# Kernel optimization log

Measured on AMD Instinct MI355X. Metric: run time of the kernel, lower is better.

The kernel has to match this reference:

```python
import jax, jax.numpy as jnp
import numpy as np

N_ITERS = 2
N_NODES = 50000
N_EDGES = 400000
NODE_DIM = 128
EDGE_DIM = 128
MLP_HIDDEN = 128


def _gru_cell(x, h, W_ih, W_hh, b_ih, b_hh):
    # torch.nn.GRUCell math. W_ih: [3H, in], W_hh: [3H, H]
    gi = x @ W_ih.T + b_ih
    gh = h @ W_hh.T + b_hh
    i_r, i_z, i_n = jnp.split(gi, 3, axis=-1)
    h_r, h_z, h_n = jnp.split(gh, 3, axis=-1)
    r = jax.nn.sigmoid(i_r + h_r)
    z = jax.nn.sigmoid(i_z + h_z)
    n = jnp.tanh(i_n + r * h_n)
    return (1.0 - z) * n + z * h


def _edge_softmax(logits, dst, num_nodes):
    # logits: [E], normalized over incoming edges of each dst node
    m = jax.ops.segment_max(logits, dst, num_segments=num_nodes)
    e = jnp.exp(logits - m[dst])
    s = jax.ops.segment_sum(e, dst, num_segments=num_nodes)
    return e / s[dst]


def setup_inputs() -> dict:
    key = jax.random.key(0)
    ks = jax.random.split(key, 20)
    s = 0.05
    inp = {
        'nf': jax.random.normal(ks[0], (N_NODES, NODE_DIM), jnp.float32),
        'ef': jax.random.normal(ks[1], (N_EDGES, EDGE_DIM), jnp.float32),
        'src': jax.random.randint(ks[2], (N_EDGES,), 0, N_NODES, jnp.int32),
        'dst': jax.random.randint(ks[3], (N_EDGES,), 0, N_NODES, jnp.int32),
        # edge GRUCell: input 2*node_dim -> hidden edge_dim
        'eW_ih': s * jax.random.normal(ks[4], (3 * EDGE_DIM, 2 * NODE_DIM), jnp.float32),
        'eW_hh': s * jax.random.normal(ks[5], (3 * EDGE_DIM, EDGE_DIM), jnp.float32),
        'eb_ih': s * jax.random.normal(ks[6], (3 * EDGE_DIM,), jnp.float32),
        'eb_hh': s * jax.random.normal(ks[7], (3 * EDGE_DIM,), jnp.float32),
        # node GRUCell: input edge_dim -> hidden node_dim
        'nW_ih': s * jax.random.normal(ks[8], (3 * NODE_DIM, EDGE_DIM), jnp.float32),
        'nW_hh': s * jax.random.normal(ks[9], (3 * NODE_DIM, NODE_DIM), jnp.float32),
        'nb_ih': s * jax.random.normal(ks[10], (3 * NODE_DIM,), jnp.float32),
        'nb_hh': s * jax.random.normal(ks[11], (3 * NODE_DIM,), jnp.float32),
        # attention MLP: edge_dim -> hidden -> 1
        'aW1': s * jax.random.normal(ks[12], (EDGE_DIM, MLP_HIDDEN), jnp.float32),
        'ab1': jnp.zeros((MLP_HIDDEN,), jnp.float32),
        'aW2': s * jax.random.normal(ks[13], (MLP_HIDDEN, 1), jnp.float32),
        'ab2': jnp.zeros((1,), jnp.float32),
    }
    return inp


def reference(nf, ef, src, dst, eW_ih, eW_hh, eb_ih, eb_hh,
              nW_ih, nW_hh, nb_ih, nb_hh, aW1, ab1, aW2, ab2):
    num_nodes = nf.shape[0]
    for _ in range(N_ITERS):
        # per-edge GRU update: input = [src_h ; dst_h], hidden = edge feature
        x_e = jnp.concatenate([nf[src], nf[dst]], axis=-1)  # [E, 2*node_dim]
        uef = _gru_cell(x_e, ef, eW_ih, eW_hh, eb_ih, eb_hh)  # [E, edge_dim]
        # attention MLP + edge softmax over destination neighborhoods
        logits = (jax.nn.relu(uef @ aW1 + ab1) @ aW2 + ab2)[:, 0]  # [E]
        attn = _edge_softmax(logits, dst, num_nodes)  # [E]
        # weighted scatter-sum aggregation to destination nodes
        agg_m = jax.ops.segment_sum(uef * attn[:, None], dst, num_segments=num_nodes)
        # node GRU update
        unf = _gru_cell(agg_m, nf, nW_ih, nW_hh, nb_ih, nb_hh)  # [N, node_dim]
        nf, ef = unf, uef
    return (nf, ef)
```

## Files before the change

kernel.cpp:

```cpp
#include <hip/hip_runtime.h>

#define NN 50000
#define NE 400000
#define DIM 128

typedef __bf16 bf16x8 __attribute__((ext_vector_type(8)));
typedef float f32x4 __attribute__((ext_vector_type(4)));
typedef unsigned short u16;

#define MFMA16 __builtin_amdgcn_mfma_f32_16x16x32_bf16

__device__ __forceinline__ u16 f2b(float f){ __bf16 b=(__bf16)f; return __builtin_bit_cast(u16,b); }
__device__ __forceinline__ float b2f(u16 h){ unsigned u = ((unsigned)h)<<16; return __builtin_bit_cast(float,u); }
__device__ __forceinline__ float sigm(float x){ return 1.0f/(1.0f+__expf(-x)); }
__device__ __forceinline__ float tanh_(float x){ float e=__expf(2.0f*x); return 1.0f-2.0f/(e+1.0f); }
__device__ __forceinline__ bf16x8 ldb8(const u16* p){ return *reinterpret_cast<const bf16x8*>(p); }

#define GLOAD_LDS(gp, lp) __builtin_amdgcn_global_load_lds( \
    (const __attribute__((address_space(1))) void*)(gp),    \
    (__attribute__((address_space(3))) void*)(lp), 16, 0, 0)

__global__ void f2b_kernel(const float* __restrict__ in, u16* __restrict__ out, int n4){
  int i = blockIdx.x*blockDim.x + threadIdx.x;
  int st = gridDim.x*blockDim.x;
  for (; i<n4; i+=st){
    float4 v = reinterpret_cast<const float4*>(in)[i];
    ushort4 o = { f2b(v.x), f2b(v.y), f2b(v.z), f2b(v.w) };
    reinterpret_cast<ushort4*>(out)[i] = o;
  }
}

__global__ void transpose128_kernel(const float* __restrict__ in, u16* __restrict__ out){
  int i = blockIdx.x*blockDim.x + threadIdx.x;
  int k = i>>7, n = i&127;
  out[n*128+k] = f2b(in[i]);
}

__global__ void zero_kernel(int* p, int n){
  int i = blockIdx.x*blockDim.x + threadIdx.x; if (i<n) p[i]=0;
}
__global__ void hist_kernel(const int* __restrict__ dst, int* __restrict__ counts, int n){
  int i = blockIdx.x*blockDim.x + threadIdx.x; if (i<n) atomicAdd(&counts[dst[i]],1);
}
__global__ void scan_kernel(const int* __restrict__ counts, int* __restrict__ rowp,
                            int* __restrict__ cursor, int n){
  __shared__ int buf[1024];
  __shared__ int run;
  const int t = threadIdx.x;
  if (t==0) run = 0;
  __syncthreads();
  for (int base=0; base<n; base+=1024){
    int v = (base+t<n) ? counts[base+t] : 0;
    buf[t]=v; __syncthreads();
    for (int off=1; off<1024; off<<=1){
      int x = (t>=off) ? buf[t-off] : 0;
      __syncthreads();
      buf[t]+=x; __syncthreads();
    }
    int incl = buf[t];
    int br = run;
    __syncthreads();
    if (base+t<n){ int ex = br+incl-v; rowp[base+t]=ex; cursor[base+t]=ex; }
    if (t==1023) run = br+incl;
    __syncthreads();
  }
  if (t==0) rowp[n]=run;
}
__global__ void scatter_kernel(const int* __restrict__ dst, int* __restrict__ cursor,
                               int* __restrict__ eids, int n){
  int i = blockIdx.x*blockDim.x + threadIdx.x;
  if (i<n){ int p = atomicAdd(&cursor[dst[i]],1); eids[p]=i; }
}

__global__ __launch_bounds__(256, 2)
void edge_kernel(const int* __restrict__ src, const int* __restrict__ dst,
                 const u16* __restrict__ nfb, u16* __restrict__ efb,
                 const u16* __restrict__ Wih, const u16* __restrict__ Whh,
                 const float* __restrict__ bih, const float* __restrict__ bhh,
                 const u16* __restrict__ aW1T, const float* __restrict__ ab1,
                 const float* __restrict__ aW2, const float* __restrict__ ab2,
                 float* __restrict__ logits, float* __restrict__ ef32out)
{
  __shared__ __align__(16) u16 wbuf[36*512];
  const int wave = threadIdx.x>>6, lane = threadIdx.x&63;
  const int r16 = lane&15, kq = lane>>4;
  const long base = (long)blockIdx.x*128 + wave*32;

  auto stage = [&](int c){
    if (c < 8){
      for (int f = wave; f < 36; f += 4){
        const u16* g;
        if (f < 24){ const int gt = f>>3, s = f&7;
          g = Wih + (long)(gt*128 + c*16 + r16)*256 + s*32 + kq*8; }
        else { const int q = f-24, gt = q>>2, s = q&3;
          g = Whh + (long)(gt*128 + c*16 + r16)*128 + s*32 + kq*8; }
        GLOAD_LDS(g, wbuf + f*512);
      }
    } else {
      for (int f = wave; f < 32; f += 4){
        const int t = f>>2, s = f&3;
        GLOAD_LDS(aW1T + (long)(t*16 + r16)*128 + s*32 + kq*8, wbuf + f*512);
      }
    }
  };

  bf16x8 ag[2][8], ae[2][4];
#pragma unroll
  for (int m=0;m<2;++m){
    const long e = base + m*16 + r16;
    const u16* sp = nfb + (long)src[e]*DIM;
    const u16* dp = nfb + (long)dst[e]*DIM;
    const u16* ep = efb + e*DIM;
#pragma unroll
    for (int s=0;s<4;++s){
      ag[m][s]   = ldb8(sp + s*32 + kq*8);
      ag[m][s+4] = ldb8(dp + s*32 + kq*8);
      ae[m][s]   = ldb8(ep + s*32 + kq*8);
    }
  }
  stage(0);
  __syncthreads();

  u16*  ebase = efb + (base + kq*4)*DIM + r16;
  float* fbase = ef32out ? ef32out + (base + kq*4)*DIM + r16 : nullptr;
  const float* bi0 = bih + r16;
  const float* bh0 = bhh + r16;

  const f32x4 vzero = {0.f,0.f,0.f,0.f};
  const u16* lbase = wbuf + lane*8;

#pragma unroll 1
  for (int c=0;c<8;++c){
    const int c16 = c*16;
    const float bir=bi0[c16], biz=bi0[c16+DIM], bin=bi0[c16+2*DIM];
    const float bhr=bh0[c16], bhz=bh0[c16+DIM], bhn=bh0[c16+2*DIM];
    float h0p[2][4];
#pragma unroll
    for (int m=0;m<2;++m)
#pragma unroll
      for (int r=0;r<4;++r) h0p[m][r] = b2f(ebase[(m*16+r)*DIM + c16]);

    f32x4 aR[2], aZ[2], aNi[2], aNh[2];
#pragma unroll
    for (int m=0;m<2;++m){ aR[m]=vzero; aZ[m]=vzero; aNi[m]=vzero; aNh[m]=vzero; }
#pragma unroll
    for (int s=0;s<8;++s){
      bf16x8 b0 = ldb8(lbase + ( s   )*512);
      bf16x8 b1 = ldb8(lbase + ( 8+s )*512);
      bf16x8 b2 = ldb8(lbase + (16+s )*512);
#pragma unroll
      for (int m=0;m<2;++m){
        aR[m]  = MFMA16(ag[m][s], b0, aR[m] ,0,0,0);
        aZ[m]  = MFMA16(ag[m][s], b1, aZ[m] ,0,0,0);
        aNi[m] = MFMA16(ag[m][s], b2, aNi[m],0,0,0);
      }
    }
#pragma unroll
    for (int s=0;s<4;++s){
      bf16x8 b0 = ldb8(lbase + (24+s)*512);
      bf16x8 b1 = ldb8(lbase + (28+s)*512);
      bf16x8 b2 = ldb8(lbase + (32+s)*512);
#pragma unroll
      for (int m=0;m<2;++m){
        aR[m]  = MFMA16(ae[m][s], b0, aR[m] ,0,0,0);
        aZ[m]  = MFMA16(ae[m][s], b1, aZ[m] ,0,0,0);
        aNh[m] = MFMA16(ae[m][s], b2, aNh[m],0,0,0);
      }
    }
    __syncthreads();
    stage(c+1);
#pragma unroll
    for (int m=0;m<2;++m){
#pragma unroll
      for (int r=0;r<4;++r){
        float rg = sigm(aR[m][r] + bir + bhr);
        float zg = sigm(aZ[m][r] + biz + bhz);
        float ng = tanh_(aNi[m][r] + bin + rg*(aNh[m][r] + bhn));
        float u  = (1.0f-zg)*ng + zg*h0p[m][r];
        ebase[(m*16+r)*DIM + c16] = f2b(u);
        if (fbase) fbase[(m*16+r)*DIM + c16] = u;
      }
    }
    __syncthreads();
  }

  bf16x8 ua[2][4];
#pragma unroll
  for (int m=0;m<2;++m){
    const u16* ep = efb + (base + m*16 + r16)*DIM;
#pragma unroll
    for (int s=0;s<4;++s) ua[m][s] = ldb8(ep + s*32 + kq*8);
  }
  float part[2][4] = {{0.f,0.f,0.f,0.f},{0.f,0.f,0.f,0.f}};
#pragma unroll 1
  for (int t=0;t<8;++t){
    f32x4 h[2] = {vzero, vzero};
#pragma unroll
    for (int s=0;s<4;++s){
      bf16x8 b = ldb8(lbase + (t*4+s)*512);
#pragma unroll
      for (int m=0;m<2;++m) h[m] = MFMA16(ua[m][s], b, h[m],0,0,0);
    }
    const int cc = t*16 + r16;
    const float b1 = ab1[cc], w2 = aW2[cc];
#pragma unroll
    for (int m=0;m<2;++m)
#pragma unroll
      for (int r=0;r<4;++r) part[m][r] += fmaxf(h[m][r]+b1, 0.f)*w2;
  }
#pragma unroll
  for (int off=1; off<16; off<<=1){
#pragma unroll
    for (int m=0;m<2;++m)
#pragma unroll
      for (int r=0;r<4;++r) part[m][r] += __shfl_xor(part[m][r], off, 64);
  }
  if (r16==0){
    const float b2v = ab2[0];
#pragma unroll
    for (int m=0;m<2;++m)
#pragma unroll
      for (int r=0;r<4;++r) logits[base + m*16 + kq*4 + r] = part[m][r] + b2v;
  }
}

__global__ __launch_bounds__(256)
void agg_kernel(const int* __restrict__ rowp, const int* __restrict__ eids,
                const float* __restrict__ logits, const u16* __restrict__ uefb,
                u16* __restrict__ aggb)
{
  const int wave = threadIdx.x>>6, lane = threadIdx.x&63;
  const int v = blockIdx.x*4 + wave;
  if (v>=NN) return;
  const int p0 = rowp[v], deg = rowp[v+1]-p0;
  float ax=0.f, ay=0.f;
  if (deg>0){
    float mx = -__builtin_inff();
    for (int i=lane; i<deg; i+=64) mx = fmaxf(mx, logits[eids[p0+i]]);
#pragma unroll
    for (int off=32; off; off>>=1) mx = fmaxf(mx, __shfl_xor(mx, off, 64));
    float ss = 0.f;
    for (int i=lane; i<deg; i+=64) ss += __expf(logits[eids[p0+i]] - mx);
#pragma unroll
    for (int off=32; off; off>>=1) ss += __shfl_xor(ss, off, 64);
    const float inv = 1.0f/ss;
    int i = 0;
    for (; i+2<=deg; i+=2){
      const int e0 = eids[p0+i], e1 = eids[p0+i+1];
      const float l0 = logits[e0], l1 = logits[e1];
      const unsigned q0 = *reinterpret_cast<const unsigned*>(uefb + (long)e0*DIM + lane*2);
      const unsigned q1 = *reinterpret_cast<const unsigned*>(uefb + (long)e1*DIM + lane*2);
      const float a0 = __expf(l0-mx)*inv, a1 = __expf(l1-mx)*inv;
      ax += a0*b2f((u16)q0) + a1*b2f((u16)q1);
      ay += a0*b2f((u16)(q0>>16)) + a1*b2f((u16)(q1>>16));
    }
    if (i<deg){
      const int e0 = eids[p0+i];
      const float a0 = __expf(logits[e0]-mx)*inv;
      const unsigned q0 = *reinterpret_cast<const unsigned*>(uefb + (long)e0*DIM + lane*2);
      ax += a0*b2f((u16)q0);
      ay += a0*b2f((u16)(q0>>16));
    }
  }
  unsigned pack = (unsigned)f2b(ax) | ((unsigned)f2b(ay)<<16);
  *reinterpret_cast<unsigned*>(aggb + (long)v*DIM + lane*2) = pack;
}

__global__ __launch_bounds__(512, 4)
void node_kernel(const u16* __restrict__ aggb, u16* __restrict__ nfb,
                 const float* nf32, float* unf32,
                 const u16* __restrict__ Wih, const u16* __restrict__ Whh,
                 const float* __restrict__ bih, const float* __restrict__ bhh)
{
  __shared__ __align__(16) u16 wbuf[2*24*512];
  const int wave = threadIdx.x>>6, lane = threadIdx.x&63;
  const int r16 = lane&15, kq = lane>>4;
  const long tbase = (long)blockIdx.x*128 + wave*16;
  const long v = tbase + r16;
  const long vcl = (v < NN) ? v : (NN-1);

  auto stage = [&](int c){
    if (c >= 8) return;
    u16* bufp = wbuf + (c&1)*24*512;
    for (int f = wave; f < 24; f += 8){
      const u16* g;
      if (f < 12){ const int gt = f>>2, s = f&3;
        g = Wih + (long)(gt*128 + c*16 + r16)*128 + s*32 + kq*8; }
      else { const int q = f-12, gt = q>>2, s = q&3;
        g = Whh + (long)(gt*128 + c*16 + r16)*128 + s*32 + kq*8; }
      GLOAD_LDS(g, bufp + f*512);
    }
  };

  bf16x8 xa[4], ha[4];
#pragma unroll
  for (int s=0;s<4;++s){
    xa[s] = ldb8(aggb + vcl*DIM + s*32 + kq*8);
    ha[s] = ldb8(nfb  + vcl*DIM + s*32 + kq*8);
  }
  stage(0);
  __syncthreads();

  const f32x4 vzero = {0.f,0.f,0.f,0.f};

#pragma unroll 1
  for (int c=0;c<8;++c){
    stage(c+1);
    const int oc = c*16 + r16;
    const float bir=bih[oc], biz=bih[DIM+oc], bin=bih[2*DIM+oc];
    const float bhr=bhh[oc], bhz=bhh[DIM+oc], bhn=bhh[2*DIM+oc];
    float h0p[4];
#pragma unroll
    for (int r=0;r<4;++r){
      const long rr = tbase + kq*4 + r;
      h0p[r] = (rr < NN) ? nf32[rr*DIM+oc] : 0.f;
    }
    const u16* lb = wbuf + (c&1)*24*512 + lane*8;
    f32x4 ar=vzero, az=vzero, an=vzero, hr=vzero, hz=vzero, hn=vzero;
#pragma unroll
    for (int s=0;s<4;++s){
      ar=MFMA16(xa[s], ldb8(lb + ( s   )*512), ar,0,0,0);
      az=MFMA16(xa[s], ldb8(lb + ( 4+s)*512), az,0,0,0);
      an=MFMA16(xa[s], ldb8(lb + ( 8+s)*512), an,0,0,0);
      hr=MFMA16(ha[s], ldb8(lb + (12+s)*512), hr,0,0,0);
      hz=MFMA16(ha[s], ldb8(lb + (16+s)*512), hz,0,0,0);
      hn=MFMA16(ha[s], ldb8(lb + (20+s)*512), hn,0,0,0);
    }
#pragma unroll
    for (int r=0;r<4;++r){
      const long rr = tbase + kq*4 + r;
      if (rr < NN){
        float rg = sigm(ar[r]+bir + hr[r]+bhr);
        float zg = sigm(az[r]+biz + hz[r]+bhz);
        float ng = tanh_(an[r]+bin + rg*(hn[r]+bhn));
        float u  = (1.0f-zg)*ng + zg*h0p[r];
        unf32[rr*DIM+oc] = u;
        nfb[rr*DIM+oc] = f2b(u);
      }
    }
    __syncthreads();
  }
}

extern "C" void kernel_launch(void* const* d_in, const int* in_sizes, int n_in,
                              void* d_out, int out_size, void* d_ws, size_t ws_size,
                              hipStream_t stream)
{
  const float* nf_in = (const float*)d_in[0];
  const float* ef_in = (const float*)d_in[1];
  const int*   src   = (const int*)d_in[2];
  const int*   dst   = (const int*)d_in[3];
  const float* eWih  = (const float*)d_in[4];
  const float* eWhh  = (const float*)d_in[5];
  const float* ebih  = (const float*)d_in[6];
  const float* ebhh  = (const float*)d_in[7];
  const float* nWih  = (const float*)d_in[8];
  const float* nWhh  = (const float*)d_in[9];
  const float* nbih  = (const float*)d_in[10];
  const float* nbhh  = (const float*)d_in[11];
  const float* aW1   = (const float*)d_in[12];
  const float* ab1   = (const float*)d_in[13];
  const float* aW2   = (const float*)d_in[14];
  const float* ab2   = (const float*)d_in[15];

  float* nf_out = (float*)d_out;
  float* ef_out = nf_out + (size_t)NN*DIM;

  char* p = (char*)d_ws;
  auto carve = [&](size_t bytes)->void*{ void* r = (void*)p; p += (bytes + 255) & ~(size_t)255; return r; };
  u16* efb    = (u16*)carve((size_t)NE*DIM*2);
  u16* nfb    = (u16*)carve((size_t)NN*DIM*2);
  u16* aggb   = (u16*)carve((size_t)NN*DIM*2);
  float* logits = (float*)carve((size_t)NE*4);
  int* eids   = (int*)carve((size_t)NE*4);
  int* counts = (int*)carve((size_t)NN*4);
  int* rowp   = (int*)carve((size_t)(NN+1)*4);
  int* cursor = (int*)carve((size_t)NN*4);
  u16* bWih   = (u16*)carve((size_t)384*256*2);
  u16* bWhh   = (u16*)carve((size_t)384*128*2);
  u16* bnWih  = (u16*)carve((size_t)384*128*2);
  u16* bnWhh  = (u16*)carve((size_t)384*128*2);
  u16* baW1T  = (u16*)carve((size_t)128*128*2);

  f2b_kernel<<<2048,256,0,stream>>>(nf_in, nfb, NN*DIM/4);
  f2b_kernel<<<2048,256,0,stream>>>(ef_in, efb, NE*DIM/4);
  f2b_kernel<<<96,256,0,stream>>>(eWih, bWih, 384*256/4);
  f2b_kernel<<<48,256,0,stream>>>(eWhh, bWhh, 384*128/4);
  f2b_kernel<<<48,256,0,stream>>>(nWih, bnWih, 384*128/4);
  f2b_kernel<<<48,256,0,stream>>>(nWhh, bnWhh, 384*128/4);
  transpose128_kernel<<<64,256,0,stream>>>(aW1, baW1T);

  zero_kernel<<<(NN+255)/256,256,0,stream>>>(counts, NN);
  hist_kernel<<<(NE+255)/256,256,0,stream>>>(dst, counts, NE);
  scan_kernel<<<1,1024,0,stream>>>(counts, rowp, cursor, NN);
  scatter_kernel<<<(NE+255)/256,256,0,stream>>>(dst, cursor, eids, NE);

  for (int it=0; it<2; ++it){
    const float* nf_cur = (it==0) ? nf_in : nf_out;
    float* efout32 = (it==1) ? ef_out : nullptr;
    edge_kernel<<<NE/128,256,0,stream>>>(src, dst, nfb, efb,
                                         bWih, bWhh, ebih, ebhh,
                                         baW1T, ab1, aW2, ab2, logits, efout32);
    agg_kernel<<<(NN+3)/4,256,0,stream>>>(rowp, eids, logits, efb, aggb);
    node_kernel<<<(NN+127)/128,512,0,stream>>>(aggb, nfb, nf_cur, nf_out,
                                               bnWih, bnWhh, nbih, nbhh);
  }
}
```

Baseline: 923.9 us.

## Precompute per-node input projections and gather them in edge GRU

```diff
diff --git a/kernel.cpp b/kernel.cpp
--- a/kernel.cpp
+++ b/kernel.cpp
@@ -34,6 +34,13 @@
   int i = blockIdx.x*blockDim.x + threadIdx.x;
   int k = i>>7, n = i&127;
   out[n*128+k] = f2b(in[i]);
+}
+
+__global__ void wproj_kernel(const float* __restrict__ Wih, u16* __restrict__ Wp){
+  int i = blockIdx.x*blockDim.x + threadIdx.x;
+  int row = i>>7, k = i&127;
+  float v = (row < 384) ? Wih[row*256 + k] : Wih[(row-384)*256 + 128 + k];
+  Wp[i] = f2b(v);
 }
 
 __global__ void zero_kernel(int* p, int n){
@@ -72,117 +79,120 @@
   if (i<n){ int p = atomicAdd(&cursor[dst[i]],1); eids[p]=i; }
 }
 
+__global__ __launch_bounds__(256)
+void proj_kernel(const u16* __restrict__ nfb, const u16* __restrict__ Wp,
+                 u16* __restrict__ P)
+{
+  const int wave = threadIdx.x>>6, lane = threadIdx.x&63;
+  const int r16 = lane&15, kq = lane>>4;
+  const long nb = (long)blockIdx.x*64 + wave*16;
+  if (nb >= NN) return;
+  const long vcl = (nb + r16 < NN) ? nb + r16 : NN-1;
+  bf16x8 a[4];
+#pragma unroll
+  for (int s=0;s<4;++s) a[s] = ldb8(nfb + vcl*DIM + s*32 + kq*8);
+  const f32x4 vzero = {0.f,0.f,0.f,0.f};
+#pragma unroll 1
+  for (int t=0;t<48;++t){
+    f32x4 acc = vzero;
+#pragma unroll
+    for (int s=0;s<4;++s)
+      acc = MFMA16(a[s], ldb8(Wp + (long)(t*16+r16)*128 + s*32 + kq*8), acc,0,0,0);
+#pragma unroll
+    for (int j=0;j<4;++j){
+      const long row = nb + kq*4 + j;
+      if (row < NN) P[row*768 + t*16 + r16] = f2b(acc[j]);
+    }
+  }
+}
+
 __global__ __launch_bounds__(256, 2)
 void edge_kernel(const int* __restrict__ src, const int* __restrict__ dst,
-                 const u16* __restrict__ nfb, u16* __restrict__ efb,
-                 const u16* __restrict__ Wih, const u16* __restrict__ Whh,
+                 const u16* __restrict__ P, u16* __restrict__ efb,
+                 const u16* __restrict__ Whh,
                  const float* __restrict__ bih, const float* __restrict__ bhh,
                  const u16* __restrict__ aW1T, const float* __restrict__ ab1,
                  const float* __restrict__ aW2, const float* __restrict__ ab2,
                  float* __restrict__ logits, float* __restrict__ ef32out)
 {
-  __shared__ __align__(16) u16 wbuf[36*512];
   const int wave = threadIdx.x>>6, lane = threadIdx.x&63;
   const int r16 = lane&15, kq = lane>>4;
   const long base = (long)blockIdx.x*128 + wave*32;
 
-  auto stage = [&](int c){
-    if (c < 8){
-      for (int f = wave; f < 36; f += 4){
-        const u16* g;
-        if (f < 24){ const int gt = f>>3, s = f&7;
-          g = Wih + (long)(gt*128 + c*16 + r16)*256 + s*32 + kq*8; }
-        else { const int q = f-24, gt = q>>2, s = q&3;
-          g = Whh + (long)(gt*128 + c*16 + r16)*128 + s*32 + kq*8; }
-        GLOAD_LDS(g, wbuf + f*512);
-      }
-    } else {
-      for (int f = wave; f < 32; f += 4){
-        const int t = f>>2, s = f&3;
-        GLOAD_LDS(aW1T + (long)(t*16 + r16)*128 + s*32 + kq*8, wbuf + f*512);
-      }
-    }
-  };
-
-  bf16x8 ag[2][8], ae[2][4];
+  int oS[2][4], oD[2][4];
+#pragma unroll
+  for (int m=0;m<2;++m)
+#pragma unroll
+    for (int r=0;r<4;++r){
+      const long e2 = base + m*16 + kq*4 + r;
+      oS[m][r] = src[e2]*768;
+      oD[m][r] = dst[e2]*768 + 384;
+    }
+
+  bf16x8 ae[2][4];
 #pragma unroll
   for (int m=0;m<2;++m){
-    const long e = base + m*16 + r16;
-    const u16* sp = nfb + (long)src[e]*DIM;
-    const u16* dp = nfb + (long)dst[e]*DIM;
-    const u16* ep = efb + e*DIM;
-#pragma unroll
-    for (int s=0;s<4;++s){
-      ag[m][s]   = ldb8(sp + s*32 + kq*8);
-      ag[m][s+4] = ldb8(dp + s*32 + kq*8);
-      ae[m][s]   = ldb8(ep + s*32 + kq*8);
-    }
-  }
-  stage(0);
-  __syncthreads();
+    const u16* ep = efb + (base + m*16 + r16)*DIM;
+#pragma unroll
+    for (int s=0;s<4;++s) ae[m][s] = ldb8(ep + s*32 + kq*8);
+  }
 
   u16*  ebase = efb + (base + kq*4)*DIM + r16;
   float* fbase = ef32out ? ef32out + (base + kq*4)*DIM + r16 : nullptr;
   const float* bi0 = bih + r16;
   const float* bh0 = bhh + r16;
-
   const f32x4 vzero = {0.f,0.f,0.f,0.f};
-  const u16* lbase = wbuf + lane*8;
 
 #pragma unroll 1
   for (int c=0;c<8;++c){
     const int c16 = c*16;
-    const float bir=bi0[c16], biz=bi0[c16+DIM], bin=bi0[c16+2*DIM];
-    const float bhr=bh0[c16], bhz=bh0[c16+DIM], bhn=bh0[c16+2*DIM];
+    float gs[2][3][4];
+#pragma unroll
+    for (int m=0;m<2;++m)
+#pragma unroll
+      for (int r=0;r<4;++r){
+        const u16* ps = P + oS[m][r] + c16 + r16;
+        const u16* pd = P + oD[m][r] + c16 + r16;
+        gs[m][0][r] = b2f(ps[0])   + b2f(pd[0]);
+        gs[m][1][r] = b2f(ps[128]) + b2f(pd[128]);
+        gs[m][2][r] = b2f(ps[256]) + b2f(pd[256]);
+      }
     float h0p[2][4];
 #pragma unroll
     for (int m=0;m<2;++m)
 #pragma unroll
       for (int r=0;r<4;++r) h0p[m][r] = b2f(ebase[(m*16+r)*DIM + c16]);
 
-    f32x4 aR[2], aZ[2], aNi[2], aNh[2];
-#pragma unroll
-    for (int m=0;m<2;++m){ aR[m]=vzero; aZ[m]=vzero; aNi[m]=vzero; aNh[m]=vzero; }
-#pragma unroll
-    for (int s=0;s<8;++s){
-      bf16x8 b0 = ldb8(lbase + ( s   )*512);
-      bf16x8 b1 = ldb8(lbase + ( 8+s )*512);
-      bf16x8 b2 = ldb8(lbase + (16+s )*512);
+    const u16* wrow = Whh + (long)(c16 + r16)*128 + kq*8;
+    f32x4 hR[2]={vzero,vzero}, hZ[2]={vzero,vzero}, hN[2]={vzero,vzero};
+#pragma unroll
+    for (int s=0;s<4;++s){
+      bf16x8 b0 = ldb8(wrow + s*32);
+      bf16x8 b1 = ldb8(wrow + s*32 + 128*128);
+      bf16x8 b2 = ldb8(wrow + s*32 + 256*128);
 #pragma unroll
       for (int m=0;m<2;++m){
-        aR[m]  = MFMA16(ag[m][s], b0, aR[m] ,0,0,0);
-        aZ[m]  = MFMA16(ag[m][s], b1, aZ[m] ,0,0,0);
-        aNi[m] = MFMA16(ag[m][s], b2, aNi[m],0,0,0);
+        hR[m]=MFMA16(ae[m][s], b0, hR[m],0,0,0);
+        hZ[m]=MFMA16(ae[m][s], b1, hZ[m],0,0,0);
+        hN[m]=MFMA16(ae[m][s], b2, hN[m],0,0,0);
       }
     }
-#pragma unroll
-    for (int s=0;s<4;++s){
-      bf16x8 b0 = ldb8(lbase + (24+s)*512);
-      bf16x8 b1 = ldb8(lbase + (28+s)*512);
-      bf16x8 b2 = ldb8(lbase + (32+s)*512);
-#pragma unroll
-      for (int m=0;m<2;++m){
-        aR[m]  = MFMA16(ae[m][s], b0, aR[m] ,0,0,0);
-        aZ[m]  = MFMA16(ae[m][s], b1, aZ[m] ,0,0,0);
-        aNh[m] = MFMA16(ae[m][s], b2, aNh[m],0,0,0);
-      }
-    }
-    __syncthreads();
-    stage(c+1);
-#pragma unroll
-    for (int m=0;m<2;++m){
+    const float btR = bi0[c16]+bh0[c16], btZ = bi0[c16+DIM]+bh0[c16+DIM];
+    const float bin = bi0[c16+2*DIM],   bhn = bh0[c16+2*DIM];
+#pragma unroll
+    for (int m=0;m<2;++m)
 #pragma unroll
       for (int r=0;r<4;++r){
-        float rg = sigm(aR[m][r] + bir + bhr);
-        float zg = sigm(aZ[m][r] + biz + bhz);
-        float ng = tanh_(aNi[m][r] + bin + rg*(aNh[m][r] + bhn));
+        float rg = sigm(gs[m][0][r] + hR[m][r] + btR);
+        float zg = sigm(gs[m][1][r] + hZ[m][r] + btZ);
+        float ng = tanh_(gs[m][2][r] + bin + rg*(hN[m][r] + bhn));
         float u  = (1.0f-zg)*ng + zg*h0p[m][r];
         ebase[(m*16+r)*DIM + c16] = f2b(u);
         if (fbase) fbase[(m*16+r)*DIM + c16] = u;
       }
-    }
-    __syncthreads();
-  }
+  }
+
+  asm volatile("s_waitcnt vmcnt(0)" ::: "memory");
 
   bf16x8 ua[2][4];
 #pragma unroll
@@ -197,7 +207,7 @@
     f32x4 h[2] = {vzero, vzero};
 #pragma unroll
     for (int s=0;s<4;++s){
-      bf16x8 b = ldb8(lbase + (t*4+s)*512);
+      bf16x8 b = ldb8(aW1T + (long)(t*16+r16)*128 + s*32 + kq*8);
 #pragma unroll
       for (int m=0;m<2;++m) h[m] = MFMA16(ua[m][s], b, h[m],0,0,0);
     }
@@ -371,12 +381,13 @@
   u16* efb    = (u16*)carve((size_t)NE*DIM*2);
   u16* nfb    = (u16*)carve((size_t)NN*DIM*2);
   u16* aggb   = (u16*)carve((size_t)NN*DIM*2);
+  u16* P      = (u16*)carve((size_t)NN*768*2);
   float* logits = (float*)carve((size_t)NE*4);
   int* eids   = (int*)carve((size_t)NE*4);
   int* counts = (int*)carve((size_t)NN*4);
   int* rowp   = (int*)carve((size_t)(NN+1)*4);
   int* cursor = (int*)carve((size_t)NN*4);
-  u16* bWih   = (u16*)carve((size_t)384*256*2);
+  u16* Wp     = (u16*)carve((size_t)768*128*2);
   u16* bWhh   = (u16*)carve((size_t)384*128*2);
   u16* bnWih  = (u16*)carve((size_t)384*128*2);
   u16* bnWhh  = (u16*)carve((size_t)384*128*2);
@@ -384,7 +395,7 @@
 
   f2b_kernel<<<2048,256,0,stream>>>(nf_in, nfb, NN*DIM/4);
   f2b_kernel<<<2048,256,0,stream>>>(ef_in, efb, NE*DIM/4);
-  f2b_kernel<<<96,256,0,stream>>>(eWih, bWih, 384*256/4);
+  wproj_kernel<<<384,256,0,stream>>>(eWih, Wp);
   f2b_kernel<<<48,256,0,stream>>>(eWhh, bWhh, 384*128/4);
   f2b_kernel<<<48,256,0,stream>>>(nWih, bnWih, 384*128/4);
   f2b_kernel<<<48,256,0,stream>>>(nWhh, bnWhh, 384*128/4);
@@ -398,8 +409,9 @@
   for (int it=0; it<2; ++it){
     const float* nf_cur = (it==0) ? nf_in : nf_out;
     float* efout32 = (it==1) ? ef_out : nullptr;
-    edge_kernel<<<NE/128,256,0,stream>>>(src, dst, nfb, efb,
-                                         bWih, bWhh, ebih, ebhh,
+    proj_kernel<<<(NN+63)/64,256,0,stream>>>(nfb, Wp, P);
+    edge_kernel<<<NE/128,256,0,stream>>>(src, dst, P, efb, bWhh,
+                                         ebih, ebhh,
                                          baW1T, ab1, aW2, ab2, logits, efout32);
     agg_kernel<<<(NN+3)/4,256,0,stream>>>(rowp, eids, logits, efb, aggb);
     node_kernel<<<(NN+127)/128,512,0,stream>>>(aggb, nfb, nf_cur, nf_out,
```

Measured after the change: 1.494 ms. +61.7%, slower.
